# Performance work log

Hardware: AMD Instinct MI355X
Metric: run time of the kernel (lower is better)

## Reference

```python
import jax, jax.numpy as jnp
import numpy as np

B, NF, EMB = 2048, 32, 64
FEAT_MAP_DIM = [128, 128, 128]  # split_half=True, activation=None


def setup_inputs() -> dict:
    key = jax.random.key(0)
    ks = jax.random.split(key, 7)
    inp = jax.random.normal(ks[0], (B, NF, EMB), dtype=jnp.float32)
    # conv1d_i: in_channels = H_{i-1} * NF, out_channels = FEAT_MAP_DIM[i]
    # H_0 = NF = 32; H_1 = H_2 = 128 // 2 = 64 (split_half)
    in_chs = [NF * NF, (FEAT_MAP_DIM[0] // 2) * NF, (FEAT_MAP_DIM[1] // 2) * NF]
    params = {}
    for i, (ic, oc) in enumerate(zip(in_chs, FEAT_MAP_DIM)):
        bound = 1.0 / np.sqrt(ic)  # torch Conv1d default init range
        params[f"W{i}"] = jax.random.uniform(ks[1 + 2 * i], (oc, ic), jnp.float32, -bound, bound)
        params[f"b{i}"] = jax.random.uniform(ks[2 + 2 * i], (oc,), jnp.float32, -bound, bound)
    return {"inp": inp, **params}


def reference(inp, W0, b0, W1, b1, W2, b2):
    # CIN: h_k[b,o,e] = sum_{j,z} W_k[o, j*NF+z] * h_{k-1}[b,j,e] * inp[b,z,e] + b_k[o]
    # The torch code materializes the outer product then applies a 1x1 conv;
    # the fused triple einsum below computes identical math.
    nf = inp.shape[1]
    Ws, bs = [W0, W1, W2], [b0, b1, b2]
    h = inp
    outs = []
    n_layers = len(Ws)
    for i, (W, b) in enumerate(zip(Ws, bs)):
        O, Hj = W.shape[0], h.shape[1]
        Wr = W.reshape(O, Hj, nf)  # channel index c = j*nf + z
        nxt = jnp.einsum('bjk,bzk,ojz->bok', h, inp, Wr) + b[None, :, None]
        if i != n_layers - 1:  # split_half
            h, o = nxt[:, : O // 2], nxt[:, O // 2 :]
        else:
            o = nxt
        outs.append(o)
    out = jnp.concatenate(outs, axis=1)  # (B, 64+64+128, EMB)
    return jnp.sum(out, axis=2)  # (B, 256)
```

## Files before the change

### kernel.cpp

```cpp
#include <hip/hip_runtime.h>


typedef _Float16 f16;
typedef _Float16 f16x4 __attribute__((ext_vector_type(4)));
typedef _Float16 f16x8 __attribute__((ext_vector_type(8)));
typedef float f32x4 __attribute__((ext_vector_type(4)));
typedef float f32x16 __attribute__((ext_vector_type(16)));

#define HSTR 72
#define PBS  5120

__device__ __forceinline__ f32x16 zero16() {
    f32x16 v;
#pragma unroll
    for (int i = 0; i < 16; ++i) v[i] = 0.0f;
    return v;
}

__global__ void __launch_bounds__(256)
prep_frag(const float* __restrict__ W0, const float* __restrict__ W1,
          const float* __restrict__ W2, f16* __restrict__ dst)
{
    int g = (blockIdx.x * 256 + threadIdx.x) * 8;
    const float* src; int base, KK, rbase;
    if (g < 65536)       { src = W0; base = 0;      KK = 64;  rbase = 0;  }
    else if (g < 131072) { src = W0; base = 65536;  KK = 64;  rbase = 64; }
    else if (g < 262144) { src = W1; base = 131072; KK = 128; rbase = 0;  }
    else if (g < 393216) { src = W1; base = 262144; KK = 128; rbase = 64; }
    else                 { src = W2; base = 393216; KK = 128; rbase = 0;  }
    int local = g - base;
    int frag  = local >> 9;
    int lane  = (local >> 3) & 63;
    int kk    = frag % KK;
    int mc    = frag / KK;
    int row   = rbase + mc * 32 + (lane & 31);
    int col   = kk * 16 + (lane >> 5) * 8;
    int IC    = KK * 16;
    const float* s = src + (size_t)row * IC + col;
    f16x8 o;
#pragma unroll
    for (int i = 0; i < 8; ++i) o[i] = (f16)s[i];
    *(f16x8*)(dst + g) = o;
}

__device__ __forceinline__ void p_chunk(const f16* __restrict__ hrows,
                                        const f16x8 (&pB)[4],
                                        f16* __restrict__ pdst, int t, int q)
{
    f32x16 acc = zero16();
#pragma unroll
    for (int s = 0; s < 4; ++s) {
        f16x8 a = *(const f16x8*)(hrows + t * HSTR + s * 16 + q * 8);
        acc = __builtin_amdgcn_mfma_f32_32x32x16_f16(a, pB[s], acc, 0, 0, 0);
    }
#pragma unroll
    for (int r = 0; r < 16; ++r) {
        int row = (r & 3) + 8 * (r >> 2) + 4 * q;
        pdst[row * 32 + t] = (f16)acc[r];
    }
}

template <int HJ>
__device__ __forceinline__ void h_gemm4(const f16* __restrict__ Hf,
                                        const f16* __restrict__ h0,
                                        const f16* __restrict__ h1,
                                        int lane8, int t,
                                        const f16x8 (&ip)[2][2][2],
                                        f32x16 (&acc)[2][2])
{
    acc[0][0] = zero16(); acc[0][1] = zero16();
    acc[1][0] = zero16(); acc[1][1] = zero16();
    const f16* Wp = Hf + lane8;
    f16x8 wf[2][2];
    f16   sc[2][4];
#pragma unroll
    for (int ph = 0; ph < 2; ++ph) {
        wf[ph][0] = *(const f16x8*)(Wp + (ph * 2 + 0) * 512);
        wf[ph][1] = *(const f16x8*)(Wp + (ph * 2 + 1) * 512);
        sc[ph][0] = h0[ph * HSTR + t];
        sc[ph][1] = h0[ph * HSTR + 32 + t];
        sc[ph][2] = h1[ph * HSTR + t];
        sc[ph][3] = h1[ph * HSTR + 32 + t];
    }
    for (int jj = 0; jj < HJ; jj += 2) {
#pragma unroll
        for (int ph = 0; ph < 2; ++ph) {
            f16x8 w0 = wf[ph][0], w1 = wf[ph][1];
            f16 s00 = sc[ph][0], s01 = sc[ph][1];
            f16 s10 = sc[ph][2], s11 = sc[ph][3];
            int jn = jj + ph + 2;
            if (jn > HJ - 1) jn = HJ - 1;
            wf[ph][0] = *(const f16x8*)(Wp + (jn * 2 + 0) * 512);
            wf[ph][1] = *(const f16x8*)(Wp + (jn * 2 + 1) * 512);
            sc[ph][0] = h0[jn * HSTR + t];
            sc[ph][1] = h0[jn * HSTR + 32 + t];
            sc[ph][2] = h1[jn * HSTR + t];
            sc[ph][3] = h1[jn * HSTR + 32 + t];
            acc[0][0] = __builtin_amdgcn_mfma_f32_32x32x16_f16(w0, ip[0][0][0] * s00, acc[0][0], 0, 0, 0);
            acc[0][0] = __builtin_amdgcn_mfma_f32_32x32x16_f16(w1, ip[0][1][0] * s00, acc[0][0], 0, 0, 0);
            acc[0][1] = __builtin_amdgcn_mfma_f32_32x32x16_f16(w0, ip[0][0][1] * s01, acc[0][1], 0, 0, 0);
            acc[0][1] = __builtin_amdgcn_mfma_f32_32x32x16_f16(w1, ip[0][1][1] * s01, acc[0][1], 0, 0, 0);
            acc[1][0] = __builtin_amdgcn_mfma_f32_32x32x16_f16(w0, ip[1][0][0] * s10, acc[1][0], 0, 0, 0);
            acc[1][0] = __builtin_amdgcn_mfma_f32_32x32x16_f16(w1, ip[1][1][0] * s10, acc[1][0], 0, 0, 0);
            acc[1][1] = __builtin_amdgcn_mfma_f32_32x32x16_f16(w0, ip[1][0][1] * s11, acc[1][1], 0, 0, 0);
            acc[1][1] = __builtin_amdgcn_mfma_f32_32x32x16_f16(w1, ip[1][1][1] * s11, acc[1][1], 0, 0, 0);
        }
    }
}

__device__ __forceinline__ void load_bias(const float* __restrict__ bl,
                                          float (&bve)[16], int g, int q)
{
#pragma unroll
    for (int r = 0; r < 16; ++r)
        bve[r] = bl[g * 32 + (r & 3) + 8 * (r >> 2) + 4 * q];
}

__device__ __forceinline__ void epi4(const f32x16 (&acc)[2][2],
                                     f16* __restrict__ h0d, f16* __restrict__ h1d,
                                     const float (&bve)[16], int g, int t, int q)
{
#pragma unroll
    for (int r = 0; r < 16; ++r) {
        int row = g * 32 + (r & 3) + 8 * (r >> 2) + 4 * q;
        h0d[row * HSTR + t]      = (f16)(acc[0][0][r] + bve[r]);
        h0d[row * HSTR + 32 + t] = (f16)(acc[0][1][r] + bve[r]);
        h1d[row * HSTR + t]      = (f16)(acc[1][0][r] + bve[r]);
        h1d[row * HSTR + 32 + t] = (f16)(acc[1][1][r] + bve[r]);
    }
}

__global__ void __launch_bounds__(256, 2)
cin_h(const float* __restrict__ inp, const f16* __restrict__ Wf,
      f16* __restrict__ pW,
      const float* __restrict__ b0v, const float* __restrict__ b1v)
{
    __shared__ __attribute__((aligned(16))) f16 hL[4 * 64 * HSTR];

    const int tid   = threadIdx.x;
    const int w     = tid >> 6;
    const int lane  = tid & 63;
    const int t     = lane & 31;
    const int q     = lane >> 5;
    const int lane8 = lane * 8;
    const int bp    = w & 1;
    const int g     = w >> 1;
    const int b0i   = blockIdx.x * 4;

#pragma unroll
    for (int it = 0; it < 8; ++it) {
        int idx = it * 1024 + tid * 4;
        int b = idx >> 11, rem = idx & 2047;
        int z = rem >> 6, k = rem & 63;
        f32x4 v = *(const f32x4*)(inp + (size_t)(b0i + b) * 2048 + rem);
        f16x4 h4;
        h4[0] = (f16)v[0]; h4[1] = (f16)v[1]; h4[2] = (f16)v[2]; h4[3] = (f16)v[3];
        *(f16x4*)(hL + b * 64 * HSTR + z * HSTR + k) = h4;
    }
    __syncthreads();

    f16x8 ip[2][2][2];
#pragma unroll
    for (int b = 0; b < 2; ++b) {
        const f16* src = hL + (bp * 2 + b) * 64 * HSTR;
#pragma unroll
        for (int kq = 0; kq < 2; ++kq)
#pragma unroll
            for (int nh = 0; nh < 2; ++nh) {
                f16x8 v;
#pragma unroll
                for (int i = 0; i < 8; ++i)
                    v[i] = src[(kq * 16 + q * 8 + i) * HSTR + nh * 32 + t];
                ip[b][kq][nh] = v;
            }
    }
    f16x8 pB[4];
#pragma unroll
    for (int s = 0; s < 4; ++s)
        pB[s] = *(const f16x8*)(hL + w * 64 * HSTR + t * HSTR + s * 16 + q * 8);

    f16* pMy = pW + (size_t)(b0i + w) * PBS;
    const f16* H0 = Wf;
    const f16* H1 = Wf + 131072;
    f16* hA = hL + (bp * 2) * 64 * HSTR;
    f16* hB = hL + (bp * 2 + 1) * 64 * HSTR;
    f32x16 acc[2][2];
    float bve[16];

    p_chunk(hL + w * 64 * HSTR, pB, pMy, t, q);
    h_gemm4<32>(H0 + g * 64 * 512, hA, hB, lane8, t, ip, acc);
    load_bias(b0v, bve, g, q);
    __syncthreads();
    epi4(acc, hA, hB, bve, g, t, q);
    __syncthreads();

    p_chunk(hL + w * 64 * HSTR,             pB, pMy + 1024, t, q);
    p_chunk(hL + w * 64 * HSTR + 32 * HSTR, pB, pMy + 2048, t, q);
    h_gemm4<64>(H1 + g * 128 * 512, hA, hB, lane8, t, ip, acc);
    load_bias(b1v, bve, g, q);
    __syncthreads();
    epi4(acc, hA, hB, bve, g, t, q);
    __syncthreads();

    p_chunk(hL + w * 64 * HSTR,             pB, pMy + 3072, t, q);
    p_chunk(hL + w * 64 * HSTR + 32 * HSTR, pB, pMy + 4096, t, q);
}

template <int S>
__device__ __forceinline__ void o_tile(const f16* __restrict__ Of,
                                       const f16* __restrict__ pBase,
                                       const float* __restrict__ biasp,
                                       float* __restrict__ out,
                                       float* __restrict__ rP,
                                       int bg, int colbase, int tid)
{
    const int w = tid >> 6, lane = tid & 63, t = lane & 31, q = lane >> 5;
    const int lane8 = lane * 8;
    const int mi = w & 1, ki = w >> 1;
    const f16* Ap = Of + (size_t)(mi * 2 * S + ki * S) * 512 + lane8;
    const f16* Bp = pBase + (size_t)(bg * 32 + t) * PBS + ki * S * 16 + q * 8;

    f32x16 acc = zero16();
    f16x8 af[4], bf[4];
#pragma unroll
    for (int i = 0; i < 4; ++i) {
        af[i] = *(const f16x8*)(Ap + i * 512);
        bf[i] = *(const f16x8*)(Bp + i * 16);
    }
#pragma unroll 4
    for (int s = 0; s < S; ++s) {
        int idx = s & 3;
        f16x8 a = af[idx], b = bf[idx];
        int sn = s + 4 < S ? s + 4 : S - 1;
        af[idx] = *(const f16x8*)(Ap + sn * 512);
        bf[idx] = *(const f16x8*)(Bp + sn * 16);
        acc = __builtin_amdgcn_mfma_f32_32x32x16_f16(a, b, acc, 0, 0, 0);
    }
#pragma unroll
    for (int r = 0; r < 16; ++r) {
        int m = mi * 32 + (r & 3) + 8 * (r >> 2) + 4 * q;
        rP[(ki * 32 + t) * 64 + m] = acc[r];
    }
    __syncthreads();
#pragma unroll
    for (int it = 0; it < 2; ++it) {
        int idx4 = (it * 256 + tid) * 4;
        int n = idx4 >> 6, o = idx4 & 63;
        f32x4 v0 = *(const f32x4*)(rP + n * 64 + o);
        f32x4 v1 = *(const f32x4*)(rP + (32 + n) * 64 + o);
        f32x4 bb = *(const f32x4*)(biasp + o);
        f32x4 ov;
        ov[0] = v0[0] + v1[0] + 64.0f * bb[0];
        ov[1] = v0[1] + v1[1] + 64.0f * bb[1];
        ov[2] = v0[2] + v1[2] + 64.0f * bb[2];
        ov[3] = v0[3] + v1[3] + 64.0f * bb[3];
        *(f32x4*)(out + (size_t)(bg * 32 + n) * 256 + colbase + o) = ov;
    }
}

__global__ void __launch_bounds__(256, 2)
cin_out(const f16* __restrict__ Wf, const f16* __restrict__ pW,
        const float* __restrict__ b0v, const float* __restrict__ b1v,
        const float* __restrict__ b2v, float* __restrict__ out)
{
    __shared__ __attribute__((aligned(16))) float rP[2 * 32 * 64];
    const int tid = threadIdx.x;
    const int r  = blockIdx.x & 3;
    const int bg = blockIdx.x >> 2;
    if (r == 0)
        o_tile<32>(Wf + 65536,  pW,        b0v + 64, out, rP, bg, 0,   tid);
    else if (r == 1)
        o_tile<64>(Wf + 262144, pW + 1024, b1v + 64, out, rP, bg, 64,  tid);
    else if (r == 2)
        o_tile<64>(Wf + 393216, pW + 3072, b2v,      out, rP, bg, 128, tid);
    else
        o_tile<64>(Wf + 524288, pW + 3072, b2v + 64, out, rP, bg, 192, tid);
}

extern "C" void kernel_launch(void* const* d_in, const int* in_sizes, int n_in,
                              void* d_out, int out_size, void* d_ws, size_t ws_size,
                              hipStream_t stream)
{
    const float* inp = (const float*)d_in[0];
    const float* W0  = (const float*)d_in[1];
    const float* b0  = (const float*)d_in[2];
    const float* W1  = (const float*)d_in[3];
    const float* b1  = (const float*)d_in[4];
    const float* W2  = (const float*)d_in[5];
    const float* b2  = (const float*)d_in[6];
    float* out = (float*)d_out;

    f16* Wf = (f16*)d_ws;
    f16* pW = Wf + 655360;

    prep_frag<<<320, 256, 0, stream>>>(W0, W1, W2, Wf);
    cin_h<<<512, 256, 0, stream>>>(inp, Wf, pW, b0, b1);
    cin_out<<<256, 256, 0, stream>>>(Wf, pW, b0, b1, b2, out);
}
```

Baseline: 139.4 us.

## Halve per-block batch in cin_h to raise occupancy and block count

cin_h now handles 2 batch rows per block instead of 4. Each wave computes one batch row instead of two, which halves the accumulator and input-fragment registers and halves LDS use, and the launch bound rises to 4 blocks per SM. The p_chunk work is redistributed across the two wave groups, and the grid doubles to 1024 blocks. The trade-off is that each weight fragment loaded from global memory is reused across fewer batch rows, so weight traffic per unit of work doubles.

```diff
diff --git a/kernel.cpp b/kernel.cpp
--- a/kernel.cpp
+++ b/kernel.cpp
@@ -61,49 +61,38 @@
 }
 
 template <int HJ>
-__device__ __forceinline__ void h_gemm4(const f16* __restrict__ Hf,
-                                        const f16* __restrict__ h0,
-                                        const f16* __restrict__ h1,
+__device__ __forceinline__ void h_gemm2(const f16* __restrict__ Hf,
+                                        const f16* __restrict__ h,
                                         int lane8, int t,
-                                        const f16x8 (&ip)[2][2][2],
-                                        f32x16 (&acc)[2][2])
-{
-    acc[0][0] = zero16(); acc[0][1] = zero16();
-    acc[1][0] = zero16(); acc[1][1] = zero16();
+                                        const f16x8 (&ip)[2][2],
+                                        f32x16 (&acc)[2])
+{
+    acc[0] = zero16(); acc[1] = zero16();
     const f16* Wp = Hf + lane8;
     f16x8 wf[2][2];
-    f16   sc[2][4];
+    f16   sc[2][2];
 #pragma unroll
     for (int ph = 0; ph < 2; ++ph) {
         wf[ph][0] = *(const f16x8*)(Wp + (ph * 2 + 0) * 512);
         wf[ph][1] = *(const f16x8*)(Wp + (ph * 2 + 1) * 512);
-        sc[ph][0] = h0[ph * HSTR + t];
-        sc[ph][1] = h0[ph * HSTR + 32 + t];
-        sc[ph][2] = h1[ph * HSTR + t];
-        sc[ph][3] = h1[ph * HSTR + 32 + t];
+        sc[ph][0] = h[ph * HSTR + t];
+        sc[ph][1] = h[ph * HSTR + 32 + t];
     }
     for (int jj = 0; jj < HJ; jj += 2) {
 #pragma unroll
         for (int ph = 0; ph < 2; ++ph) {
             f16x8 w0 = wf[ph][0], w1 = wf[ph][1];
-            f16 s00 = sc[ph][0], s01 = sc[ph][1];
-            f16 s10 = sc[ph][2], s11 = sc[ph][3];
+            f16 s0 = sc[ph][0], s1 = sc[ph][1];
             int jn = jj + ph + 2;
             if (jn > HJ - 1) jn = HJ - 1;
             wf[ph][0] = *(const f16x8*)(Wp + (jn * 2 + 0) * 512);
             wf[ph][1] = *(const f16x8*)(Wp + (jn * 2 + 1) * 512);
-            sc[ph][0] = h0[jn * HSTR + t];
-            sc[ph][1] = h0[jn * HSTR + 32 + t];
-            sc[ph][2] = h1[jn * HSTR + t];
-            sc[ph][3] = h1[jn * HSTR + 32 + t];
-            acc[0][0] = __builtin_amdgcn_mfma_f32_32x32x16_f16(w0, ip[0][0][0] * s00, acc[0][0], 0, 0, 0);
-            acc[0][0] = __builtin_amdgcn_mfma_f32_32x32x16_f16(w1, ip[0][1][0] * s00, acc[0][0], 0, 0, 0);
-            acc[0][1] = __builtin_amdgcn_mfma_f32_32x32x16_f16(w0, ip[0][0][1] * s01, acc[0][1], 0, 0, 0);
-            acc[0][1] = __builtin_amdgcn_mfma_f32_32x32x16_f16(w1, ip[0][1][1] * s01, acc[0][1], 0, 0, 0);
-            acc[1][0] = __builtin_amdgcn_mfma_f32_32x32x16_f16(w0, ip[1][0][0] * s10, acc[1][0], 0, 0, 0);
-            acc[1][0] = __builtin_amdgcn_mfma_f32_32x32x16_f16(w1, ip[1][1][0] * s10, acc[1][0], 0, 0, 0);
-            acc[1][1] = __builtin_amdgcn_mfma_f32_32x32x16_f16(w0, ip[1][0][1] * s11, acc[1][1], 0, 0, 0);
-            acc[1][1] = __builtin_amdgcn_mfma_f32_32x32x16_f16(w1, ip[1][1][1] * s11, acc[1][1], 0, 0, 0);
+            sc[ph][0] = h[jn * HSTR + t];
+            sc[ph][1] = h[jn * HSTR + 32 + t];
+            acc[0] = __builtin_amdgcn_mfma_f32_32x32x16_f16(w0, ip[0][0] * s0, acc[0], 0, 0, 0);
+            acc[0] = __builtin_amdgcn_mfma_f32_32x32x16_f16(w1, ip[1][0] * s0, acc[0], 0, 0, 0);
+            acc[1] = __builtin_amdgcn_mfma_f32_32x32x16_f16(w0, ip[0][1] * s1, acc[1], 0, 0, 0);
+            acc[1] = __builtin_amdgcn_mfma_f32_32x32x16_f16(w1, ip[1][1] * s1, acc[1], 0, 0, 0);
         }
     }
 }
@@ -116,26 +105,24 @@
         bve[r] = bl[g * 32 + (r & 3) + 8 * (r >> 2) + 4 * q];
 }
 
-__device__ __forceinline__ void epi4(const f32x16 (&acc)[2][2],
-                                     f16* __restrict__ h0d, f16* __restrict__ h1d,
+__device__ __forceinline__ void epi2(const f32x16 (&acc)[2],
+                                     f16* __restrict__ hd,
                                      const float (&bve)[16], int g, int t, int q)
 {
 #pragma unroll
     for (int r = 0; r < 16; ++r) {
         int row = g * 32 + (r & 3) + 8 * (r >> 2) + 4 * q;
-        h0d[row * HSTR + t]      = (f16)(acc[0][0][r] + bve[r]);
-        h0d[row * HSTR + 32 + t] = (f16)(acc[0][1][r] + bve[r]);
-        h1d[row * HSTR + t]      = (f16)(acc[1][0][r] + bve[r]);
-        h1d[row * HSTR + 32 + t] = (f16)(acc[1][1][r] + bve[r]);
-    }
-}
-
-__global__ void __launch_bounds__(256, 2)
+        hd[row * HSTR + t]      = (f16)(acc[0][r] + bve[r]);
+        hd[row * HSTR + 32 + t] = (f16)(acc[1][r] + bve[r]);
+    }
+}
+
+__global__ void __launch_bounds__(256, 4)
 cin_h(const float* __restrict__ inp, const f16* __restrict__ Wf,
       f16* __restrict__ pW,
       const float* __restrict__ b0v, const float* __restrict__ b1v)
 {
-    __shared__ __attribute__((aligned(16))) f16 hL[4 * 64 * HSTR];
+    __shared__ __attribute__((aligned(16))) f16 hL[2 * 64 * HSTR];
 
     const int tid   = threadIdx.x;
     const int w     = tid >> 6;
@@ -143,67 +130,62 @@
     const int t     = lane & 31;
     const int q     = lane >> 5;
     const int lane8 = lane * 8;
-    const int bp    = w & 1;
+    const int b     = w & 1;
     const int g     = w >> 1;
-    const int b0i   = blockIdx.x * 4;
-
-#pragma unroll
-    for (int it = 0; it < 8; ++it) {
+    const int b0i   = blockIdx.x * 2;
+
+#pragma unroll
+    for (int it = 0; it < 4; ++it) {
         int idx = it * 1024 + tid * 4;
-        int b = idx >> 11, rem = idx & 2047;
+        int bb = idx >> 11, rem = idx & 2047;
         int z = rem >> 6, k = rem & 63;
-        f32x4 v = *(const f32x4*)(inp + (size_t)(b0i + b) * 2048 + rem);
+        f32x4 v = *(const f32x4*)(inp + (size_t)(b0i + bb) * 2048 + rem);
         f16x4 h4;
         h4[0] = (f16)v[0]; h4[1] = (f16)v[1]; h4[2] = (f16)v[2]; h4[3] = (f16)v[3];
-        *(f16x4*)(hL + b * 64 * HSTR + z * HSTR + k) = h4;
-    }
-    __syncthreads();
-
-    f16x8 ip[2][2][2];
-#pragma unroll
-    for (int b = 0; b < 2; ++b) {
-        const f16* src = hL + (bp * 2 + b) * 64 * HSTR;
-#pragma unroll
-        for (int kq = 0; kq < 2; ++kq)
-#pragma unroll
-            for (int nh = 0; nh < 2; ++nh) {
-                f16x8 v;
-#pragma unroll
-                for (int i = 0; i < 8; ++i)
-                    v[i] = src[(kq * 16 + q * 8 + i) * HSTR + nh * 32 + t];
-                ip[b][kq][nh] = v;
-            }
-    }
+        *(f16x4*)(hL + bb * 64 * HSTR + z * HSTR + k) = h4;
+    }
+    __syncthreads();
+
+    f16* hD = hL + b * 64 * HSTR;
+
+    f16x8 ip[2][2];
+#pragma unroll
+    for (int kq = 0; kq < 2; ++kq)
+#pragma unroll
+        for (int nh = 0; nh < 2; ++nh) {
+            f16x8 v;
+#pragma unroll
+            for (int i = 0; i < 8; ++i)
+                v[i] = hD[(kq * 16 + q * 8 + i) * HSTR + nh * 32 + t];
+            ip[kq][nh] = v;
+        }
     f16x8 pB[4];
 #pragma unroll
     for (int s = 0; s < 4; ++s)
-        pB[s] = *(const f16x8*)(hL + w * 64 * HSTR + t * HSTR + s * 16 + q * 8);
-
-    f16* pMy = pW + (size_t)(b0i + w) * PBS;
+        pB[s] = *(const f16x8*)(hD + t * HSTR + s * 16 + q * 8);
+
+    f16* pMy = pW + (size_t)(b0i + b) * PBS;
     const f16* H0 = Wf;
     const f16* H1 = Wf + 131072;
-    f16* hA = hL + (bp * 2) * 64 * HSTR;
-    f16* hB = hL + (bp * 2 + 1) * 64 * HSTR;
-    f32x16 acc[2][2];
+    f32x16 acc[2];
     float bve[16];
 
-    p_chunk(hL + w * 64 * HSTR, pB, pMy, t, q);
-    h_gemm4<32>(H0 + g * 64 * 512, hA, hB, lane8, t, ip, acc);
+    if (g == 0)
+        p_chunk(hD, pB, pMy, t, q);
+    h_gemm2<32>(H0 + g * 64 * 512, hD, lane8, t, ip, acc);
     load_bias(b0v, bve, g, q);
     __syncthreads();
-    epi4(acc, hA, hB, bve, g, t, q);
-    __syncthreads();
-
-    p_chunk(hL + w * 64 * HSTR,             pB, pMy + 1024, t, q);
-    p_chunk(hL + w * 64 * HSTR + 32 * HSTR, pB, pMy + 2048, t, q);
-    h_gemm4<64>(H1 + g * 128 * 512, hA, hB, lane8, t, ip, acc);
+    epi2(acc, hD, bve, g, t, q);
+    __syncthreads();
+
+    p_chunk(hD + g * 32 * HSTR, pB, pMy + 1024 + g * 1024, t, q);
+    h_gemm2<64>(H1 + g * 128 * 512, hD, lane8, t, ip, acc);
     load_bias(b1v, bve, g, q);
     __syncthreads();
-    epi4(acc, hA, hB, bve, g, t, q);
-    __syncthreads();
-
-    p_chunk(hL + w * 64 * HSTR,             pB, pMy + 3072, t, q);
-    p_chunk(hL + w * 64 * HSTR + 32 * HSTR, pB, pMy + 4096, t, q);
+    epi2(acc, hD, bve, g, t, q);
+    __syncthreads();
+
+    p_chunk(hD + g * 32 * HSTR, pB, pMy + 3072 + g * 1024, t, q);
 }
 
 template <int S>
@@ -294,6 +276,6 @@
     f16* pW = Wf + 655360;
 
     prep_frag<<<320, 256, 0, stream>>>(W0, W1, W2, Wf);
-    cin_h<<<512, 256, 0, stream>>>(inp, Wf, pW, b0, b1);
+    cin_h<<<1024, 256, 0, stream>>>(inp, Wf, pW, b0, b1);
     cin_out<<<256, 256, 0, stream>>>(Wf, pW, b0, b1, b2, out);
 }
```

After: 147.9 us. 1.06x slower.
